# Optimization experiments

Hardware: AMD Instinct MI355X
Metric: run time of the kernel (lower is better)

## Reference

```python
import jax, jax.numpy as jnp
import numpy as np

N = 1024          # number of rois (single image)
C = 1024          # in_channels
G = 16            # num_groups
PE = 64           # position_embedding_channels
WAVE_LENGTH = 1000.0


def _position_embedding(bboxes, pe_channels, wave_length):
    # bboxes: [N, 4] xyxy. Pairwise geometric features vs all (nongt == all) boxes.
    x1, y1, x2, y2 = jnp.split(bboxes, 4, axis=1)          # each [N,1]
    cx = (x1 + x2) * 0.5
    cy = (y1 + y2) * 0.5
    w = x2 - x1 + 1.0
    h = y2 - y1 + 1.0
    dX = jnp.log(jnp.clip(jnp.abs((cx - cx.T) / w), 1e-3))  # [N,N]
    dY = jnp.log(jnp.clip(jnp.abs((cy - cy.T) / h), 1e-3))
    dW = jnp.log(w / w.T)
    dH = jnp.log(h / h.T)
    pm = jnp.stack([dX, dY, dW, dH], axis=-1)               # [N,N,4]
    feat_range = jnp.arange(pe_channels // 8, dtype=pm.dtype)
    dim_mat = jnp.power(jnp.asarray(wave_length, pm.dtype),
                        (8.0 / pe_channels) * feat_range)    # [pe//8]
    div = (100.0 * pm)[..., None] / dim_mat                  # [N,N,4,pe//8]
    emb = jnp.concatenate([jnp.sin(div), jnp.cos(div)], axis=3)  # [N,N,4,pe//4]
    return emb.reshape(emb.shape[0], emb.shape[1], -1)       # [N,N,pe]


def setup_inputs() -> dict:
    key = jax.random.key(0)
    ks = jax.random.split(key, 10)
    feats = jax.random.normal(ks[0], (N, C), dtype=jnp.float32)
    # realistic boxes: x1,y1 in [0,800), w,h in [1,200)
    x1 = jax.random.uniform(ks[1], (N, 1), minval=0.0, maxval=800.0)
    y1 = jax.random.uniform(ks[2], (N, 1), minval=0.0, maxval=800.0)
    bw = jax.random.uniform(ks[3], (N, 1), minval=1.0, maxval=200.0)
    bh = jax.random.uniform(ks[4], (N, 1), minval=1.0, maxval=200.0)
    rois = jnp.concatenate([jnp.zeros((N, 1)), x1, y1, x1 + bw, y1 + bh], axis=1).astype(jnp.float32)
    Wq = 0.01 * jax.random.normal(ks[5], (C, C), dtype=jnp.float32)
    bq = jnp.zeros((C,), jnp.float32)
    Wk = 0.01 * jax.random.normal(ks[6], (C, C), dtype=jnp.float32)
    bk = jnp.zeros((C,), jnp.float32)
    Wg = 0.01 * jax.random.normal(ks[7], (G, PE), dtype=jnp.float32)   # 1x1 conv PE->G
    bg = jnp.zeros((G,), jnp.float32)
    # grouped 1x1 conv: in=G*C, out=C, groups=G -> weight [C, C]
    limit = np.sqrt(6.0 / (C + C))
    Wv = jax.random.uniform(ks[8], (C, C), minval=-limit, maxval=limit, dtype=jnp.float32)
    bv = jnp.zeros((C,), jnp.float32)
    return {"feats": feats, "rois": rois, "Wq": Wq, "bq": bq, "Wk": Wk, "bk": bk,
            "Wg": Wg, "bg": bg, "Wv": Wv, "bv": bv}


def reference(feats, rois, Wq, bq, Wk, bk, Wg, bg, Wv, bv):
    n, c = feats.shape
    g = Wg.shape[0]
    gc = c // g
    # position embedding computed under no_grad in torch
    emb = jax.lax.stop_gradient(_position_embedding(rois[:, 1:5], Wg.shape[1], WAVE_LENGTH))  # [N,N,PE]
    # 1x1 conv w_g + relu -> geometric attention weight [N, G, M]
    aff_weight = jax.nn.relu(jnp.einsum('nmp,gp->ngm', emb, Wg) + bg[None, :, None])
    q = (feats @ Wq.T + bq).reshape(n, g, gc)   # [N,G,gc]
    k = (feats @ Wk.T + bk).reshape(n, g, gc)   # [M,G,gc] (nongt == all)
    scale = 1.0 / jnp.sqrt(jnp.asarray(gc, jnp.float32))
    aff = jnp.einsum('ngc,mgc->ngm', q, k) * scale            # [N,G,M]
    weighted = jnp.log(jnp.clip(aff_weight, 1e-6)) + aff
    sm = jax.nn.softmax(weighted, axis=2)                      # [N,G,M]
    out = jnp.einsum('ngm,mc->ngc', sm, feats)                 # [N,G,C]
    # grouped 1x1 conv w_v: group g maps its C-dim aggregate to gc channels
    Wv_g = Wv.reshape(g, gc, c)
    rel = jnp.einsum('ngc,gdc->ngd', out, Wv_g).reshape(n, c) + bv
    return rel
```

## Files before the change

### kernel.cpp

```cpp
#include <hip/hip_runtime.h>
#include <math.h>

#define N_ROIS 1024
#define C_DIM  1024

typedef __attribute__((ext_vector_type(8))) short short8;
typedef __attribute__((ext_vector_type(4))) float f32x4;

__device__ __forceinline__ unsigned short f2bf(float x) {
    union { float f; unsigned u; } v; v.f = x;
    unsigned r = v.u + 0x7fffu + ((v.u >> 16) & 1u);
    return (unsigned short)(r >> 16);
}
__device__ __forceinline__ float bf2f(unsigned short u) {
    return __uint_as_float((unsigned)u << 16);
}
__device__ __forceinline__ unsigned cvtpk(float lo, float hi) {
    unsigned r;
    asm("v_cvt_pk_bf16_f32 %0, %1, %2" : "=v"(r) : "v"(lo), "v"(hi));
    return r;
}

__global__ __launch_bounds__(256) void cvt_kernel(
    const float* __restrict__ s0, const float* __restrict__ s1,
    const float* __restrict__ s2, const float* __restrict__ s3,
    unsigned short* __restrict__ d0, unsigned short* __restrict__ d1,
    unsigned short* __restrict__ d2, unsigned short* __restrict__ d3)
{
    const float* s; unsigned short* d;
    switch (blockIdx.y) {
        case 0:  s = s0; d = d0; break;
        case 1:  s = s1; d = d1; break;
        case 2:  s = s2; d = d2; break;
        default: s = s3; d = d3; break;
    }
    const int i = (blockIdx.x * 256 + threadIdx.x) * 8;
    float4 a = *(const float4*)&s[i];
    float4 b = *(const float4*)&s[i + 4];
    uint4 o;
    o.x = cvtpk(a.x, a.y); o.y = cvtpk(a.z, a.w);
    o.z = cvtpk(b.x, b.y); o.w = cvtpk(b.z, b.w);
    *(uint4*)&d[i] = o;
}

struct Triples {
    const unsigned short* A[3];
    const unsigned short* B[3];
    unsigned short*       C[3];
    const float*          bias[3];
};

__global__ __launch_bounds__(256) void prep_kernel(
    Triples tr, const float* __restrict__ rois, const float* __restrict__ Wg,
    const float* __restrict__ bg, unsigned short* __restrict__ logw)
{
    __shared__ __align__(16) char smem[24576];
    const int bx = blockIdx.x;
    const int t  = threadIdx.x;
    const int grp = bx / 11, rem = bx % 11;

    if (rem < 3) {
        const int gid = grp * 3 + rem;
        const int z   = gid >> 7;
        const int r3  = gid & 127;
        const int m0 = (r3 >> 3) * 64, n0 = (r3 & 7) * 128;
        const unsigned short* A = tr.A[z];
        const unsigned short* B = tr.B[z];

        const int lane = t & 63, w = t >> 6;
        const int lx = lane & 15, qw = lane >> 4;

#define PGLD(srcp, dstoff) __builtin_amdgcn_global_load_lds( \
        (const __attribute__((address_space(1))) void*)(srcp), \
        (__attribute__((address_space(3))) void*)(smem + (dstoff)), 16, 0, 0)

        const int rsub = lane >> 2;
        const int sg   = ((lane & 3) ^ (rsub & 3)) * 8;
#define STAGE(bb, kk) do { \
        PGLD(A + (size_t)(m0 + w * 16 + rsub) * 1024 + (kk) + sg, \
             (bb) * 4096 + w * 1024 + lane * 16); \
        PGLD(B + (size_t)(n0 + w * 32 + rsub) * 1024 + (kk) + sg, \
             8192 + (bb) * 8192 + (w * 2) * 1024 + lane * 16); \
        PGLD(B + (size_t)(n0 + w * 32 + 16 + rsub) * 1024 + (kk) + sg, \
             8192 + (bb) * 8192 + (w * 2 + 1) * 1024 + lane * 16); \
    } while (0)

        f32x4 acc[2][4];
        const f32x4 z4 = {0.f, 0.f, 0.f, 0.f};
#pragma unroll
        for (int i = 0; i < 2; ++i)
#pragma unroll
            for (int j = 0; j < 4; ++j) acc[i][j] = z4;

        const int wm = (w & 1) * 32, wn = (w >> 1) * 64;
        const int rdsw = (qw ^ (lx & 3)) << 4;

        STAGE(0, 0);
        __syncthreads();

        for (int k0 = 0; k0 < 1024; k0 += 32) {
            const int cur = (k0 >> 5) & 1;
            if (k0 + 32 < 1024) STAGE(cur ^ 1, k0 + 32);
            const char* Ac = smem + cur * 4096;
            const char* Bc = smem + 8192 + cur * 8192;
            short8 af[2], bfr[4];
#pragma unroll
            for (int mi = 0; mi < 2; ++mi)
                af[mi] = *(const short8*)(Ac + (wm + mi * 16 + lx) * 64 + rdsw);
#pragma unroll
            for (int ni = 0; ni < 4; ++ni)
                bfr[ni] = *(const short8*)(Bc + (wn + ni * 16 + lx) * 64 + rdsw);
#pragma unroll
            for (int mi = 0; mi < 2; ++mi)
#pragma unroll
                for (int ni = 0; ni < 4; ++ni)
                    acc[mi][ni] = __builtin_amdgcn_mfma_f32_16x16x32_bf16(
                        af[mi], bfr[ni], acc[mi][ni], 0, 0, 0);
            __syncthreads();
        }
#undef STAGE
#undef PGLD

        const float* bias = tr.bias[z];
        unsigned short* C = tr.C[z];
        const float sc = (z == 0) ? 0.125f : 1.0f;
        const int r0 = qw * 4, cc = lx;
#pragma unroll
        for (int mi = 0; mi < 2; ++mi)
#pragma unroll
            for (int ni = 0; ni < 4; ++ni) {
                const int col = n0 + wn + ni * 16 + cc;
                const float bb = bias ? bias[col] : 0.f;
                const int rowi = m0 + wm + mi * 16 + r0;
                const unsigned p01 = cvtpk((acc[mi][ni][0] + bb) * sc,
                                           (acc[mi][ni][1] + bb) * sc);
                const unsigned p23 = cvtpk((acc[mi][ni][2] + bb) * sc,
                                           (acc[mi][ni][3] + bb) * sc);
                C[(size_t)rowi * 1024 + col]       = (unsigned short)(p01 & 0xffff);
                C[(size_t)(rowi + 1) * 1024 + col] = (unsigned short)(p01 >> 16);
                C[(size_t)(rowi + 2) * 1024 + col] = (unsigned short)(p23 & 0xffff);
                C[(size_t)(rowi + 3) * 1024 + col] = (unsigned short)(p23 >> 16);
            }
    } else {
        unsigned short* wg_s = (unsigned short*)smem;
        float* bg_s = (float*)(smem + 2304);
        float (*mbox)[4] = (float(*)[4])(smem + 2368);
        unsigned short* ptile0 = (unsigned short*)(smem + 6464);
        const int pb = grp * 8 + (rem - 3);
        const int ngrp = pb >> 2;
        const int mc   = (pb & 3) * 256;
        const int lane = t & 63, w = t >> 6;
        const int g = lane & 15, qw = lane >> 4;
        unsigned short* pt = ptile0 + w * 2240;

        if (t < 128) {
            const int gi = t >> 3, c = (t & 7) * 8;
            unsigned short* d = &wg_s[gi * 72 + c];
#pragma unroll
            for (int u2 = 0; u2 < 8; ++u2) d[u2] = f2bf(Wg[gi * 64 + c + u2]);
        }
        if (t < 16) bg_s[t] = bg[t];
        {
            const int m = mc + t;
            const float x1 = rois[m * 5 + 1], y1 = rois[m * 5 + 2];
            const float x2 = rois[m * 5 + 3], y2 = rois[m * 5 + 4];
            mbox[t][0] = (x1 + x2) * 0.5f;
            mbox[t][1] = (y1 + y2) * 0.5f;
            mbox[t][2] = __logf(x2 - x1 + 1.f);
            mbox[t][3] = __logf(y2 - y1 + 1.f);
        }
        const int n = ngrp * 4 + w;
        const float x1 = rois[n * 5 + 1], y1 = rois[n * 5 + 2];
        const float x2 = rois[n * 5 + 3], y2 = rois[n * 5 + 4];
        const float cxn = (x1 + x2) * 0.5f, cyn = (y1 + y2) * 0.5f;
        const float wn = x2 - x1 + 1.f, hn = y2 - y1 + 1.f;
        const float iwn = 1.f / wn, ihn = 1.f / hn;
        const float lwn = __logf(wn), lhn = __logf(hn);
        __syncthreads();

        const float coff = (qw & 1) ? 1.5707963268f : 0.f;
        const int f0 = qw >> 1;
        const short8 bf0 = *(const short8*)&wg_s[g * 72 + qw * 8];
        const short8 bf1 = *(const short8*)&wg_s[g * 72 + qw * 8 + 32];
        const float bgv = bg_s[g];
        const float invd[8] = {1.f, 0.42169650342f, 0.1778279410f, 0.07498942093f,
                               0.0316227766f, 0.01333521432f, 0.005623413252f, 0.002371373706f};

        for (int cl = 0; cl < 16; ++cl) {
            float4 mb = *(const float4*)&mbox[cl * 16 + g][0];
            float p0 = (f0 == 0)
                     ? __logf(fmaxf(fabsf((cxn - mb.x) * iwn), 1e-3f))
                     : __logf(fmaxf(fabsf((cyn - mb.y) * ihn), 1e-3f));
            float p1 = (f0 == 0) ? (lwn - mb.z) : (lhn - mb.w);
            p0 *= 100.f; p1 *= 100.f;
            float s0v[8], s1v[8];
#pragma unroll
            for (int rr = 0; rr < 8; ++rr) {
                s0v[rr] = __sinf(p0 * invd[rr] + coff);
                s1v[rr] = __sinf(p1 * invd[rr] + coff);
            }
            union { uint4 u; short8 s; } a0, a1;
            a0.u.x = cvtpk(s0v[0], s0v[1]); a0.u.y = cvtpk(s0v[2], s0v[3]);
            a0.u.z = cvtpk(s0v[4], s0v[5]); a0.u.w = cvtpk(s0v[6], s0v[7]);
            a1.u.x = cvtpk(s1v[0], s1v[1]); a1.u.y = cvtpk(s1v[2], s1v[3]);
            a1.u.z = cvtpk(s1v[4], s1v[5]); a1.u.w = cvtpk(s1v[6], s1v[7]);
            f32x4 acc = {0.f, 0.f, 0.f, 0.f};
            acc = __builtin_amdgcn_mfma_f32_16x16x32_bf16(a0.s, bf0, acc, 0, 0, 0);
            acc = __builtin_amdgcn_mfma_f32_16x16x32_bf16(a1.s, bf1, acc, 0, 0, 0);
            const float l0 = __logf(fmaxf(acc[0] + bgv, 1e-6f));
            const float l1 = __logf(fmaxf(acc[1] + bgv, 1e-6f));
            const float l2 = __logf(fmaxf(acc[2] + bgv, 1e-6f));
            const float l3 = __logf(fmaxf(acc[3] + bgv, 1e-6f));
            uint2 pk;
            pk.x = cvtpk(l0, l1);
            pk.y = cvtpk(l2, l3);
            *(uint2*)&pt[g * 140 + (cl & 7) * 16 + qw * 4] = pk;

            if ((cl & 7) == 7) {
                const int fl = cl >> 3;
                const int gg = lane >> 2, c4 = lane & 3;
                unsigned short* op = logw + (size_t)n * 16384 + gg * 1024 + mc + fl * 128;
                const unsigned short* rp = &pt[gg * 140];
#pragma unroll
                for (int j = 0; j < 8; ++j) {
                    const int mo = (c4 + j * 4) * 4;
                    *(uint2*)&op[mo] = *(const uint2*)&rp[mo];
                }
            }
        }
    }
}

#define QOFF 0
#define KOFF 8192
#define FOFF 24576
#define LOFF 40960
#define POFF 57344
#define PPAD 72

__global__ __launch_bounds__(256) void attn_kernel(
    const unsigned short* __restrict__ qb, const unsigned short* __restrict__ kb,
    const unsigned short* __restrict__ logw, const unsigned short* __restrict__ FWt,
    const float* __restrict__ bv, float* __restrict__ out)
{
    __shared__ __align__(16) char smem[66560];

    const int t = threadIdx.x;
    const int bid = blockIdx.x;
    const int g  = (bid & 7) * 2 + ((bid >> 3) >> 4);
    const int n0 = ((bid >> 3) & 15) * 64;

    const int lane = t & 63, W = t >> 6;
    const int qw = lane >> 4, lx = lane & 15;
    const int lx7 = lx & 7;
    const int r8 = lane >> 3, u = lane & 7;

#define GLD(srcp, ldsoff) __builtin_amdgcn_global_load_lds( \
        (const __attribute__((address_space(1))) void*)(srcp), \
        (__attribute__((address_space(3))) void*)(smem + (ldsoff)), 16, 0, 0)

#pragma unroll
    for (int j = 0; j < 2; ++j) {
        const int c = W * 2 + j;
        const int r = c * 8 + r8;
        GLD(qb + (size_t)(n0 + r) * 1024 + g * 64 + ((u ^ (r & 7)) * 8),
            QOFF + c * 1024);
        GLD(kb + (size_t)r * 1024 + g * 64 + ((u ^ (r & 7)) * 8),
            KOFF + c * 1024);
        GLD(FWt + (size_t)(g * 64 + r) * 1024 + ((u ^ (r & 7)) * 8),
            FOFF + c * 1024);
        GLD(logw + (size_t)(n0 + r) * 16384 + g * 1024 + (((2 * u) ^ (r & 6)) * 4),
            LOFF + c * 1024);
    }
    __syncthreads();

    const unsigned short* qS = (const unsigned short*)(smem + QOFF);
    const int qrow = W * 16 + lx;
    const short8 bq0 = *(const short8*)(qS + qrow * 64 + ((qw ^ lx7) * 8));
    const short8 bq1 = *(const short8*)(qS + qrow * 64 + (((qw + 4) ^ lx7) * 8));
    unsigned short* Pw = (unsigned short*)(smem + POFF) + W * 16 * PPAD;

    f32x4 acc[4];
    const f32x4 z4 = {0.f, 0.f, 0.f, 0.f};
#pragma unroll
    for (int nb = 0; nb < 4; ++nb) acc[nb] = z4;
    float mrow = -1e30f, srow = 0.f;

    for (int i = 0; i < 16; ++i) {
        const int cur = i & 1;
        if (i < 15) {
            const int mc = (i + 1) * 64;
            const int nxt = cur ^ 1;
#pragma unroll
            for (int j = 0; j < 2; ++j) {
                const int c = W * 2 + j;
                const int r = c * 8 + r8;
                GLD(kb + (size_t)(mc + r) * 1024 + g * 64 + ((u ^ (r & 7)) * 8),
                    KOFF + nxt * 8192 + c * 1024);
                GLD(FWt + (size_t)(g * 64 + r) * 1024 + mc + ((u ^ (r & 7)) * 8),
                    FOFF + nxt * 8192 + c * 1024);
                GLD(logw + (size_t)(n0 + r) * 16384 + g * 1024 + mc
                        + (((2 * u) ^ (r & 6)) * 4),
                    LOFF + nxt * 8192 + c * 1024);
            }
        }

        const unsigned short* Kc = (const unsigned short*)(smem + KOFF + cur * 8192);
        const unsigned short* Fc = (const unsigned short*)(smem + FOFF + cur * 8192);
        const unsigned short* Lc = (const unsigned short*)(smem + LOFF + cur * 8192);

        f32x4 s[4];
#pragma unroll
        for (int tt = 0; tt < 4; ++tt) {
            const unsigned short* kr = Kc + (tt * 16 + lx) * 64;
            short8 a0 = *(const short8*)(kr + ((qw ^ lx7) * 8));
            short8 a1 = *(const short8*)(kr + (((qw + 4) ^ lx7) * 8));
            f32x4 z = z4;
            z = __builtin_amdgcn_mfma_f32_16x16x32_bf16(a0, bq0, z, 0, 0, 0);
            s[tt] = __builtin_amdgcn_mfma_f32_16x16x32_bf16(a1, bq1, z, 0, 0, 0);
        }

        const unsigned short* Lr = Lc + (W * 16 + lx) * 64;
        float v[4][4];
        float cmx = -1e30f;
#pragma unroll
        for (int tt = 0; tt < 4; ++tt) {
            const int off = ((tt * 32 + qw * 8) ^ ((lx & 6) << 3)) >> 1;
            const uint2 lw = *(const uint2*)(Lr + off);
            v[tt][0] = s[tt][0] + bf2f((unsigned short)(lw.x & 0xffff));
            v[tt][1] = s[tt][1] + bf2f((unsigned short)(lw.x >> 16));
            v[tt][2] = s[tt][2] + bf2f((unsigned short)(lw.y & 0xffff));
            v[tt][3] = s[tt][3] + bf2f((unsigned short)(lw.y >> 16));
            cmx = fmaxf(cmx, fmaxf(fmaxf(v[tt][0], v[tt][1]), fmaxf(v[tt][2], v[tt][3])));
        }
        cmx = fmaxf(cmx, __shfl_xor(cmx, 16));
        cmx = fmaxf(cmx, __shfl_xor(cmx, 32));

        const float nm = fmaxf(mrow, cmx);
        const float f  = __expf(mrow - nm);
        mrow = nm;
        srow *= f;
#pragma unroll
        for (int nb = 0; nb < 4; ++nb) {
            acc[nb][0] *= f; acc[nb][1] *= f;
            acc[nb][2] *= f; acc[nb][3] *= f;
        }

#pragma unroll
        for (int tt = 0; tt < 4; ++tt) {
            const float p0 = __expf(v[tt][0] - nm);
            const float p1 = __expf(v[tt][1] - nm);
            const float p2 = __expf(v[tt][2] - nm);
            const float p3 = __expf(v[tt][3] - nm);
            srow += (p0 + p1) + (p2 + p3);
            uint2 pk;
            pk.x = cvtpk(p0, p1);
            pk.y = cvtpk(p2, p3);
            *(uint2*)&Pw[lx * PPAD + tt * 16 + qw * 4] = pk;
        }

#pragma unroll
        for (int ks = 0; ks < 2; ++ks) {
            const short8 ap = *(const short8*)&Pw[lx * PPAD + ks * 32 + qw * 8];
#pragma unroll
            for (int nb = 0; nb < 4; ++nb) {
                const unsigned short* fr = Fc + (nb * 16 + lx) * 64;
                short8 fb = *(const short8*)(fr + (((ks * 4 + qw) ^ lx7) * 8));
                acc[nb] = __builtin_amdgcn_mfma_f32_16x16x32_bf16(fb, ap, acc[nb], 0, 0, 0);
            }
        }

        __syncthreads();
    }

    srow += __shfl_xor(srow, 16);
    srow += __shfl_xor(srow, 32);
    const float inv = 1.f / srow;
    float* Ow = (float*)smem + W * 16 * 68;
#pragma unroll
    for (int nb = 0; nb < 4; ++nb)
#pragma unroll
        for (int r = 0; r < 4; ++r)
            Ow[lx * 68 + nb * 16 + qw * 4 + r] = acc[nb][r] * inv;
    {
        const int row = lane >> 2, d0 = (lane & 3) * 16;
        const float* Orow = (float*)smem + W * 16 * 68 + row * 68;
        float* op = out + (size_t)(n0 + W * 16 + row) * 1024 + g * 64 + d0;
#pragma unroll
        for (int j = 0; j < 4; ++j) {
            float4 o = *(const float4*)(Orow + d0 + j * 4);
            const float4 b4 = *(const float4*)&bv[g * 64 + d0 + j * 4];
            o.x += b4.x; o.y += b4.y; o.z += b4.z; o.w += b4.w;
            *(float4*)(op + j * 4) = o;
        }
    }
#undef GLD
}

extern "C" void kernel_launch(void* const* d_in, const int* in_sizes, int n_in,
                              void* d_out, int out_size, void* d_ws, size_t ws_size,
                              hipStream_t stream)
{
    const float* feats = (const float*)d_in[0];
    const float* rois  = (const float*)d_in[1];
    const float* Wq    = (const float*)d_in[2];
    const float* bq    = (const float*)d_in[3];
    const float* Wk    = (const float*)d_in[4];
    const float* bk    = (const float*)d_in[5];
    const float* Wg    = (const float*)d_in[6];
    const float* bg    = (const float*)d_in[7];
    const float* Wv    = (const float*)d_in[8];
    const float* bv    = (const float*)d_in[9];
    float* out = (float*)d_out;

    char* wsb = (char*)d_ws;
    unsigned short* logwb  = (unsigned short*)(wsb + (0ull  << 20));
    unsigned short* featsb = (unsigned short*)(wsb + (64ull << 20));
    unsigned short* qb     = (unsigned short*)(wsb + (66ull << 20));
    unsigned short* kb     = (unsigned short*)(wsb + (68ull << 20));
    unsigned short* FWtb   = (unsigned short*)(wsb + (70ull << 20));
    unsigned short* Wqb    = (unsigned short*)(wsb + (80ull << 20));
    unsigned short* Wkb    = (unsigned short*)(wsb + (82ull << 20));
    unsigned short* Wvb    = (unsigned short*)(wsb + (84ull << 20));

    cvt_kernel<<<dim3(512, 4), 256, 0, stream>>>(feats, Wq, Wk, Wv,
                                                 featsb, Wqb, Wkb, Wvb);

    Triples tr;
    tr.A[0] = featsb; tr.B[0] = Wqb;    tr.C[0] = qb;   tr.bias[0] = bq;
    tr.A[1] = featsb; tr.B[1] = Wkb;    tr.C[1] = kb;   tr.bias[1] = bk;
    tr.A[2] = Wvb;    tr.B[2] = featsb; tr.C[2] = FWtb; tr.bias[2] = nullptr;
    prep_kernel<<<1408, 256, 0, stream>>>(tr, rois, Wg, bg, logwb);

    attn_kernel<<<256, 256, 0, stream>>>(qb, kb, logwb, FWtb, bv, out);
}
```

Before: 60.77 us.

## Use single-buffered K=128 tiles in prep GEMM instead of double-buffered K=32

The prep kernel's GEMM path now stages 128-wide K slices of A and B into LDS with an XOR swizzle. It runs four MFMA substeps per barrier pair instead of double-buffering 32-wide slices. This cuts the number of barriers and loop iterations by a factor of four. In exchange it drops overlap of global loads with compute and doubles LDS use to 48KB, which may lower occupancy for the other block roles sharing this kernel.

```diff
diff --git a/kernel.cpp b/kernel.cpp
--- a/kernel.cpp
+++ b/kernel.cpp
@@ -54,7 +54,7 @@
     Triples tr, const float* __restrict__ rois, const float* __restrict__ Wg,
     const float* __restrict__ bg, unsigned short* __restrict__ logw)
 {
-    __shared__ __align__(16) char smem[24576];
+    __shared__ __align__(16) char smem[49152];
     const int bx = blockIdx.x;
     const int t  = threadIdx.x;
     const int grp = bx / 11, rem = bx % 11;
@@ -69,22 +69,13 @@
 
         const int lane = t & 63, w = t >> 6;
         const int lx = lane & 15, qw = lane >> 4;
+        const int rsub4 = lane >> 4;
+        const int c16   = lane & 15;
 
 #define PGLD(srcp, dstoff) __builtin_amdgcn_global_load_lds( \
         (const __attribute__((address_space(1))) void*)(srcp), \
         (__attribute__((address_space(3))) void*)(smem + (dstoff)), 16, 0, 0)
 
-        const int rsub = lane >> 2;
-        const int sg   = ((lane & 3) ^ (rsub & 3)) * 8;
-#define STAGE(bb, kk) do { \
-        PGLD(A + (size_t)(m0 + w * 16 + rsub) * 1024 + (kk) + sg, \
-             (bb) * 4096 + w * 1024 + lane * 16); \
-        PGLD(B + (size_t)(n0 + w * 32 + rsub) * 1024 + (kk) + sg, \
-             8192 + (bb) * 8192 + (w * 2) * 1024 + lane * 16); \
-        PGLD(B + (size_t)(n0 + w * 32 + 16 + rsub) * 1024 + (kk) + sg, \
-             8192 + (bb) * 8192 + (w * 2 + 1) * 1024 + lane * 16); \
-    } while (0)
-
         f32x4 acc[2][4];
         const f32x4 z4 = {0.f, 0.f, 0.f, 0.f};
 #pragma unroll
@@ -93,32 +84,41 @@
             for (int j = 0; j < 4; ++j) acc[i][j] = z4;
 
         const int wm = (w & 1) * 32, wn = (w >> 1) * 64;
-        const int rdsw = (qw ^ (lx & 3)) << 4;
-
-        STAGE(0, 0);
-        __syncthreads();
-
-        for (int k0 = 0; k0 < 1024; k0 += 32) {
-            const int cur = (k0 >> 5) & 1;
-            if (k0 + 32 < 1024) STAGE(cur ^ 1, k0 + 32);
-            const char* Ac = smem + cur * 4096;
-            const char* Bc = smem + 8192 + cur * 8192;
-            short8 af[2], bfr[4];
-#pragma unroll
-            for (int mi = 0; mi < 2; ++mi)
-                af[mi] = *(const short8*)(Ac + (wm + mi * 16 + lx) * 64 + rdsw);
-#pragma unroll
-            for (int ni = 0; ni < 4; ++ni)
-                bfr[ni] = *(const short8*)(Bc + (wn + ni * 16 + lx) * 64 + rdsw);
-#pragma unroll
-            for (int mi = 0; mi < 2; ++mi)
+
+        for (int k0 = 0; k0 < 1024; k0 += 128) {
+#pragma unroll
+            for (int j = 0; j < 4; ++j) {
+                const int r = w * 16 + j * 4 + rsub4;
+                PGLD(A + (size_t)(m0 + r) * 1024 + k0 + ((c16 ^ (r & 15)) * 8),
+                     w * 4096 + j * 1024);
+            }
+#pragma unroll
+            for (int j = 0; j < 8; ++j) {
+                const int r = w * 32 + j * 4 + rsub4;
+                PGLD(B + (size_t)(n0 + r) * 1024 + k0 + ((c16 ^ (r & 15)) * 8),
+                     16384 + w * 8192 + j * 1024);
+            }
+            __syncthreads();
+
+#pragma unroll
+            for (int ks = 0; ks < 4; ++ks) {
+                const int csl = ((ks * 4 + qw) ^ lx) * 16;
+                short8 af[2], bfr[4];
+#pragma unroll
+                for (int mi = 0; mi < 2; ++mi)
+                    af[mi] = *(const short8*)(smem + (wm + mi * 16 + lx) * 256 + csl);
 #pragma unroll
                 for (int ni = 0; ni < 4; ++ni)
-                    acc[mi][ni] = __builtin_amdgcn_mfma_f32_16x16x32_bf16(
-                        af[mi], bfr[ni], acc[mi][ni], 0, 0, 0);
+                    bfr[ni] = *(const short8*)(smem + 16384 + (wn + ni * 16 + lx) * 256 + csl);
+#pragma unroll
+                for (int mi = 0; mi < 2; ++mi)
+#pragma unroll
+                    for (int ni = 0; ni < 4; ++ni)
+                        acc[mi][ni] = __builtin_amdgcn_mfma_f32_16x16x32_bf16(
+                            af[mi], bfr[ni], acc[mi][ni], 0, 0, 0);
+            }
             __syncthreads();
         }
-#undef STAGE
 #undef PGLD
 
         const float* bias = tr.bias[z];
```

Result: slower. 62.82 us (+3.4%).
